# Kernel optimization log

Hardware: AMD Instinct MI355X
Metric: run time of the kernel (lower is better)

## Reference

```python
import jax, jax.numpy as jnp
import numpy as np

N_HEAD = 16
INPUT_DIM = 1024
D_K = 64


def setup_inputs() -> dict:
    key = jax.random.key(0)
    k1, k2, k3 = jax.random.split(key, 3)
    x = jax.random.normal(k1, (4, 2048, INPUT_DIM), dtype=jnp.float32)
    # xavier_uniform for linear weights
    def xavier(k, shape):
        fan_out, fan_in = shape
        limit = (6.0 / (fan_in + fan_out)) ** 0.5
        return jax.random.uniform(k, shape, jnp.float32, -limit, limit)
    W_qkv = xavier(k2, (3 * D_K * N_HEAD, INPUT_DIM))
    b_qkv = jnp.zeros((3 * D_K * N_HEAD,), jnp.float32)
    W_o = xavier(k3, (D_K * N_HEAD, D_K * N_HEAD))
    b_o = jnp.zeros((D_K * N_HEAD,), jnp.float32)
    return {"x": x, "W_qkv": W_qkv, "b_qkv": b_qkv, "W_o": W_o, "b_o": b_o}


def reference(x, W_qkv, b_qkv, W_o, b_o):
    B, S, _ = x.shape
    h = x @ W_qkv.T + b_qkv                      # (B, S, 3*d_k*H)
    # NOTE: original module reshapes directly (no transpose) to (B, H, S, 3*d_k)
    h = h.reshape(B, N_HEAD, S, 3 * D_K)
    q, k, v = jnp.split(h, 3, axis=-1)           # each (B, H, S, d_k)
    scores = jnp.einsum("bhqd,bhkd->bhqk", q, k) / jnp.sqrt(jnp.float32(D_K))
    attn = jax.nn.softmax(scores, axis=-1)       # (B, H, S, S)
    o = jnp.einsum("bhqk,bhkd->bhqd", attn, v)   # (B, H, S, d_k)
    o = o.transpose(0, 2, 1, 3).reshape(B, S, N_HEAD * D_K)
    return o @ W_o.T + b_o
```

## Files before the change

### kernel.cpp

```cpp
#include <hip/hip_runtime.h>
#include <stdint.h>


typedef __attribute__((ext_vector_type(8))) short short8;
typedef __attribute__((ext_vector_type(4))) short short4v;
typedef __attribute__((ext_vector_type(4))) float f32x4;
typedef __attribute__((ext_vector_type(16))) float f32x16;

#define B_SZ 4
#define S_SZ 2048
#define H_N 16
#define DK 64
#define IN_DIM 1024
#define QKV_DIM 3072
#define MODEL 1024
#define M_ROWS (B_SZ * S_SZ)

#define QSCALE 0.1803368801f

#if __has_builtin(__builtin_amdgcn_exp2f)
#define EXP2(x) __builtin_amdgcn_exp2f(x)
#else
#define EXP2(x) exp2f(x)
#endif

__device__ __forceinline__ short f2bf(float f) {
    union { float f; uint32_t u; } v; v.f = f;
    uint32_t r = v.u + 0x7FFFu + ((v.u >> 16) & 1u);
    return (short)(r >> 16);
}

__device__ __forceinline__ uint32_t pk2f(float a, float b) {
    uint32_t r;
    asm("v_cvt_pk_bf16_f32 %0, %1, %2" : "=v"(r) : "v"(a), "v"(b));
    return r;
}

__device__ __forceinline__ void gld_lds16(const void* g, void* l) {
    __builtin_amdgcn_global_load_lds(
        (const __attribute__((address_space(1))) void*)g,
        (__attribute__((address_space(3))) void*)l, 16, 0, 0);
}

__global__ __launch_bounds__(256) void cvt_kernel(
    const float* __restrict__ x, const float* __restrict__ wq,
    const float* __restrict__ wo, short* __restrict__ xb,
    short* __restrict__ wqb, short* __restrict__ wob) {
    const int NX = M_ROWS * IN_DIM / 4;
    const int NQ = QKV_DIM * IN_DIM / 4;
    const int NO = MODEL * IN_DIM / 4;
    const int total = NX + NQ + NO;
    for (int i = blockIdx.x * blockDim.x + threadIdx.x; i < total;
         i += gridDim.x * blockDim.x) {
        const f32x4* src; short4v* dst; int j;
        if (i < NX)           { src = (const f32x4*)x;  dst = (short4v*)xb;  j = i; }
        else if (i < NX + NQ) { src = (const f32x4*)wq; dst = (short4v*)wqb; j = i - NX; }
        else                  { src = (const f32x4*)wo; dst = (short4v*)wob; j = i - NX - NQ; }
        f32x4 v = src[j];
        short4v o;
        o[0] = f2bf(v[0]); o[1] = f2bf(v[1]); o[2] = f2bf(v[2]); o[3] = f2bf(v[3]);
        dst[j] = o;
    }
}

__global__ __launch_bounds__(512, 1) void gemm_big(
    const short* __restrict__ A, const short* __restrict__ Bm,
    const float* __restrict__ bias,
    short* __restrict__ Qb, short* __restrict__ Kb, short* __restrict__ Vt,
    int M, int N, int K) {
    __shared__ short As[4][256 * 32];
    __shared__ short Bs[4][256 * 32];
    const int tid = threadIdx.x;
    const int wave = tid >> 6, lane = tid & 63;
    const int row16 = lane & 15, kgrp = lane >> 4;
    const int wrbase = (wave >> 2) * 128;
    const int wcbase = (wave & 3) * 64;
    const int nwg = gridDim.x * gridDim.y;
    const int id = blockIdx.y * gridDim.x + blockIdx.x;
    const int nid = (id & 7) * (nwg >> 3) + (id >> 3);
    const int bn = nid % gridDim.x, bm = nid / gridDim.x;
    const short* Ab = A + (size_t)bm * 256 * K;
    const short* Bb = Bm + (size_t)bn * 256 * K;
    f32x4 acc[8][4] = {};

    const int srow = wave * 16 + (lane >> 2);
    const int soff = ((lane & 3) ^ ((lane >> 3) & 3)) * 8;
    const short* ag0 = Ab + (size_t)srow * K + soff;
    const short* ag1 = Ab + (size_t)(srow + 128) * K + soff;
    const short* bg0 = Bb + (size_t)srow * K + soff;
    const short* bg1 = Bb + (size_t)(srow + 128) * K + soff;
#define GSTAGE(BUF, K0)                                                        \
    {                                                                          \
        gld_lds16(ag0 + (K0), &As[BUF][(wave * 16) * 32]);                     \
        gld_lds16(ag1 + (K0), &As[BUF][(wave * 16 + 128) * 32]);               \
        gld_lds16(bg0 + (K0), &Bs[BUF][(wave * 16) * 32]);                     \
        gld_lds16(bg1 + (K0), &Bs[BUF][(wave * 16 + 128) * 32]);               \
    }
    const int NK = K >> 5;
    GSTAGE(0, 0);
    GSTAGE(1, 32);
    GSTAGE(2, 64);
    const int rch = (kgrp ^ ((row16 >> 1) & 3)) * 8;
    for (int t = 0; t < NK; ++t) {
        if (t + 2 < NK)      asm volatile("s_waitcnt vmcnt(8)" ::: "memory");
        else if (t + 1 < NK) asm volatile("s_waitcnt vmcnt(4)" ::: "memory");
        else                 asm volatile("s_waitcnt vmcnt(0)" ::: "memory");
        __builtin_amdgcn_s_barrier();
        __builtin_amdgcn_sched_barrier(0);
        const int cur = t & 3;
        const int nb = (t + 3) & 3;
        if (t + 3 < NK) {
            gld_lds16(ag0 + (t + 3) * 32, &As[nb][(wave * 16) * 32]);
            gld_lds16(ag1 + (t + 3) * 32, &As[nb][(wave * 16 + 128) * 32]);
        }
        short8 bf[4];
#pragma unroll
        for (int j = 0; j < 4; ++j)
            bf[j] = *(const short8*)&Bs[cur][(wcbase + j * 16 + row16) * 32 + rch];
        __builtin_amdgcn_s_setprio(1);
#pragma unroll
        for (int i = 0; i < 4; ++i) {
            short8 af = *(const short8*)&As[cur][(wrbase + i * 16 + row16) * 32 + rch];
#pragma unroll
            for (int j = 0; j < 4; ++j)
                acc[i][j] = __builtin_amdgcn_mfma_f32_16x16x32_bf16(
                    af, bf[j], acc[i][j], 0, 0, 0);
        }
        __builtin_amdgcn_s_setprio(0);
        if (t + 3 < NK) {
            gld_lds16(bg0 + (t + 3) * 32, &Bs[nb][(wave * 16) * 32]);
            gld_lds16(bg1 + (t + 3) * 32, &Bs[nb][(wave * 16 + 128) * 32]);
        }
        __builtin_amdgcn_s_setprio(1);
#pragma unroll
        for (int i = 4; i < 8; ++i) {
            short8 af = *(const short8*)&As[cur][(wrbase + i * 16 + row16) * 32 + rch];
#pragma unroll
            for (int j = 0; j < 4; ++j)
                acc[i][j] = __builtin_amdgcn_mfma_f32_16x16x32_bf16(
                    af, bf[j], acc[i][j], 0, 0, 0);
        }
        __builtin_amdgcn_s_setprio(0);
    }
#undef GSTAGE
#pragma unroll
    for (int j = 0; j < 4; ++j) {
        int gcol = bn * 256 + wcbase + j * 16 + row16;
        float bv = bias[gcol];
#pragma unroll
        for (int i = 0; i < 8; ++i) {
#pragma unroll
            for (int r = 0; r < 4; ++r) {
                int grow = bm * 256 + wrbase + i * 16 + kgrp * 4 + r;
                float val = acc[i][j][r] + bv;
                int b = grow >> 11, so = grow & 2047;
                int hh = so >> 7, a = so & 127;
                int rr = gcol / 192, cc = gcol - rr * 192;
                int ss = a * 16 + rr;
                int bh = b * H_N + hh;
                if (cc < 64) {
                    Qb[(((size_t)bh) * S_SZ + ss) * DK + cc] = f2bf(val * QSCALE);
                } else if (cc < 128) {
                    Kb[(((size_t)bh) * S_SZ + ss) * DK + cc - 64] = f2bf(val);
                } else {
                    Vt[((size_t)bh * DK + (cc - 128)) * S_SZ + ss] = f2bf(val);
                }
            }
        }
    }
}

template <int MODE>
__global__ __launch_bounds__(256, 2) void gemm_bt(
    const short* __restrict__ A, const short* __restrict__ Bm,
    const float* __restrict__ bias, float* __restrict__ Cout,
    short* __restrict__ Qb, short* __restrict__ Kb, short* __restrict__ Vt,
    int M, int N, int K) {
    __shared__ short As[3][128 * 32];
    __shared__ short Bs[3][128 * 32];
    const int tid = threadIdx.x;
    const int wave = tid >> 6, lane = tid & 63;
    const int row16 = lane & 15, kgrp = lane >> 4;
    const int wm = (wave >> 1) * 64, wn = (wave & 1) * 64;
    const int nwg = gridDim.x * gridDim.y;
    const int id = blockIdx.y * gridDim.x + blockIdx.x;
    const int nid = (id & 7) * (nwg >> 3) + (id >> 3);
    const int bn = nid % gridDim.x, bm = nid / gridDim.x;
    const short* Ab = A + (size_t)bm * 128 * K;
    const short* Bb = Bm + (size_t)bn * 128 * K;
    f32x4 acc[4][4] = {};

    const int srow = wave * 16 + (lane >> 2);
    const int soff = ((lane & 3) ^ ((srow >> 1) & 3)) * 8;
    const short* ag0 = Ab + (size_t)srow * K + soff;
    const short* ag1 = Ab + (size_t)(srow + 64) * K + soff;
    const short* bg0 = Bb + (size_t)srow * K + soff;
    const short* bg1 = Bb + (size_t)(srow + 64) * K + soff;
#define GSTAGE(BUF, K0)                                                        \
    {                                                                          \
        gld_lds16(ag0 + (K0), &As[BUF][(wave * 16) * 32]);                     \
        gld_lds16(ag1 + (K0), &As[BUF][(wave * 16 + 64) * 32]);                \
        gld_lds16(bg0 + (K0), &Bs[BUF][(wave * 16) * 32]);                     \
        gld_lds16(bg1 + (K0), &Bs[BUF][(wave * 16 + 64) * 32]);                \
    }

    const int NK = K >> 5;
    GSTAGE(0, 0);
    GSTAGE(1, 32);
    const int rch = (kgrp ^ ((row16 >> 1) & 3)) * 8;
    int cur = 0;
    for (int t = 0; t < NK; ++t) {
        if (t + 1 < NK) asm volatile("s_waitcnt vmcnt(4)" ::: "memory");
        else            asm volatile("s_waitcnt vmcnt(0)" ::: "memory");
        __builtin_amdgcn_s_barrier();
        __builtin_amdgcn_sched_barrier(0);
        if (t + 2 < NK) {
            int nb = cur + 2; if (nb >= 3) nb -= 3;
            GSTAGE(nb, (t + 2) * 32);
        }
        short8 af[4], bfr[4];
#pragma unroll
        for (int i = 0; i < 4; ++i)
            af[i] = *(const short8*)&As[cur][(wm + i * 16 + row16) * 32 + rch];
#pragma unroll
        for (int j = 0; j < 4; ++j)
            bfr[j] = *(const short8*)&Bs[cur][(wn + j * 16 + row16) * 32 + rch];
        __builtin_amdgcn_s_setprio(1);
#pragma unroll
        for (int i = 0; i < 4; ++i)
#pragma unroll
            for (int j = 0; j < 4; ++j)
                acc[i][j] = __builtin_amdgcn_mfma_f32_16x16x32_bf16(
                    af[i], bfr[j], acc[i][j], 0, 0, 0);
        __builtin_amdgcn_s_setprio(0);
        ++cur; if (cur == 3) cur = 0;
    }
#undef GSTAGE
#pragma unroll
    for (int j = 0; j < 4; ++j) {
        int gcol = bn * 128 + wn + j * 16 + row16;
        float bv = bias[gcol];
#pragma unroll
        for (int i = 0; i < 4; ++i) {
#pragma unroll
            for (int r = 0; r < 4; ++r) {
                int grow = bm * 128 + wm + i * 16 + kgrp * 4 + r;
                float val = acc[i][j][r] + bv;
                if (MODE == 1) {
                    Cout[(size_t)grow * N + gcol] = val;
                } else {
                    int b = grow >> 11, so = grow & 2047;
                    int hh = so >> 7, a = so & 127;
                    int rr = gcol / 192, cc = gcol - rr * 192;
                    int ss = a * 16 + rr;
                    int bh = b * H_N + hh;
                    if (cc < 64) {
                        Qb[(((size_t)bh) * S_SZ + ss) * DK + cc] = f2bf(val * QSCALE);
                    } else if (cc < 128) {
                        Kb[(((size_t)bh) * S_SZ + ss) * DK + cc - 64] = f2bf(val);
                    } else {
                        Vt[((size_t)bh * DK + (cc - 128)) * S_SZ + ss] = f2bf(val);
                    }
                }
            }
        }
    }
}

__global__ __launch_bounds__(256, 3) void attn_kernel(
    const short* __restrict__ Qg, const short* __restrict__ Kg,
    const short* __restrict__ Vtg, short* __restrict__ O) {
    __shared__ short Ks[2][64 * 64];
    __shared__ short Vs[2][64 * 64];
    const int tid = threadIdx.x;
    const int wave = tid >> 6, lane = tid & 63;
    const int q = lane & 31, hi = lane >> 5;
    const int id = blockIdx.x;
    const int bh = (id & 7) * 8 + ((id >> 3) & 7);
    const int qt = id >> 6;
    const int b = bh >> 4, h = bh & 15;
    const short* Qp = Qg + (size_t)bh * S_SZ * DK;
    const short* Kp = Kg + (size_t)bh * S_SZ * DK;
    const short* Vp = Vtg + (size_t)bh * DK * S_SZ;
    const int q0 = qt * 128 + wave * 32;

    short8 qf[4];
#pragma unroll
    for (int c = 0; c < 4; ++c)
        qf[c] = *(const short8*)&Qp[(size_t)(q0 + q) * DK + c * 16 + hi * 8];

    f32x16 ot0 = {}, ot1 = {};
    float m_run = -1e30f, l_run = 0.f;

    const int srow0 = wave * 16 + (lane >> 3);
    const int srow1 = srow0 + 8;
    const int sc0 = ((lane & 7) ^ (srow0 & 7)) * 8;
    const int sc1 = ((lane & 7) ^ (srow1 & 7)) * 8;
    const short* kg0 = Kp + (size_t)srow0 * DK + sc0;
    const short* kg1 = Kp + (size_t)srow1 * DK + sc1;
    const short* vg0 = Vp + (size_t)srow0 * S_SZ + sc0;
    const short* vg1 = Vp + (size_t)srow1 * S_SZ + sc1;
#define STAGE(BUF)                                                              \
    {                                                                           \
        gld_lds16(kg0, &Ks[BUF][(wave * 16) * 64]);                             \
        gld_lds16(kg1, &Ks[BUF][(wave * 16 + 8) * 64]);                         \
        gld_lds16(vg0, &Vs[BUF][(wave * 16) * 64]);                             \
        gld_lds16(vg1, &Vs[BUF][(wave * 16 + 8) * 64]);                         \
        kg0 += 64 * DK; kg1 += 64 * DK; vg0 += 64; vg1 += 64;                   \
    }

    STAGE(0);

    const int NT = S_SZ / 64;
    for (int t = 0; t < NT; ++t) {
        __syncthreads();
        const int cur = t & 1;
        if (t + 1 < NT) STAGE(cur ^ 1);

        const int qx = (q & 7) << 3;
        f32x16 st0 = {}, st1 = {};
        __builtin_amdgcn_s_setprio(1);
#pragma unroll
        for (int c = 0; c < 4; ++c) {
            const int sw = (((c * 2 + hi) << 3) ^ qx);
            short8 kf0 = *(const short8*)&Ks[cur][q * 64 + sw];
            short8 kf1 = *(const short8*)&Ks[cur][(32 + q) * 64 + sw];
            st0 = __builtin_amdgcn_mfma_f32_32x32x16_bf16(kf0, qf[c], st0, 0, 0, 0);
            st1 = __builtin_amdgcn_mfma_f32_32x32x16_bf16(kf1, qf[c], st1, 0, 0, 0);
        }
        __builtin_amdgcn_s_setprio(0);

        float ma = fmaxf(fmaxf(st0[0], st0[1]), st0[2]);
        float mb = fmaxf(fmaxf(st0[8], st0[9]), st0[10]);
        float mc = fmaxf(fmaxf(st1[0], st1[1]), st1[2]);
        float md = fmaxf(fmaxf(st1[8], st1[9]), st1[10]);
        ma = fmaxf(fmaxf(ma, st0[3]), st0[4]);
        mb = fmaxf(fmaxf(mb, st0[11]), st0[12]);
        mc = fmaxf(fmaxf(mc, st1[3]), st1[4]);
        md = fmaxf(fmaxf(md, st1[11]), st1[12]);
        ma = fmaxf(fmaxf(ma, st0[5]), st0[6]);
        mb = fmaxf(fmaxf(mb, st0[13]), st0[14]);
        mc = fmaxf(fmaxf(mc, st1[5]), st1[6]);
        md = fmaxf(fmaxf(md, st1[13]), st1[14]);
        ma = fmaxf(ma, st0[7]);
        mb = fmaxf(mb, st0[15]);
        mc = fmaxf(mc, st1[7]);
        md = fmaxf(md, st1[15]);
        float pm = fmaxf(fmaxf(ma, mb), fmaxf(mc, md));
        pm = fmaxf(pm, __shfl_xor(pm, 32));
        if (__any(pm > m_run + 8.f)) {
            float mnew = fmaxf(m_run, pm);
            float corr = EXP2(m_run - mnew);
            m_run = mnew;
            l_run *= corr;
#pragma unroll
            for (int r = 0; r < 16; ++r) { ot0[r] *= corr; ot1[r] *= corr; }
        }
        float s0 = 0.f, s1 = 0.f, s2 = 0.f, s3 = 0.f;
#pragma unroll
        for (int r = 0; r < 16; r += 4) {
            st0[r] = EXP2(st0[r] - m_run);         s0 += st0[r];
            st0[r + 1] = EXP2(st0[r + 1] - m_run); s1 += st0[r + 1];
            st0[r + 2] = EXP2(st0[r + 2] - m_run); s2 += st0[r + 2];
            st0[r + 3] = EXP2(st0[r + 3] - m_run); s3 += st0[r + 3];
        }
#pragma unroll
        for (int r = 0; r < 16; r += 4) {
            st1[r] = EXP2(st1[r] - m_run);         s0 += st1[r];
            st1[r + 1] = EXP2(st1[r + 1] - m_run); s1 += st1[r + 1];
            st1[r + 2] = EXP2(st1[r + 2] - m_run); s2 += st1[r + 2];
            st1[r + 3] = EXP2(st1[r + 3] - m_run); s3 += st1[r + 3];
        }
        float ssum = (s0 + s1) + (s2 + s3);
        ssum += __shfl_xor(ssum, 32);
        l_run += ssum;

        __builtin_amdgcn_s_setprio(1);
#if __has_builtin(__builtin_amdgcn_permlane32_swap)
#define PVCHUNK(ST, B0, CH)                                                    \
    {                                                                          \
        uint32_t A01 = pk2f(ST[(B0) + 0], ST[(B0) + 1]);                       \
        uint32_t A23 = pk2f(ST[(B0) + 2], ST[(B0) + 3]);                       \
        uint32_t B45 = pk2f(ST[(B0) + 4], ST[(B0) + 5]);                       \
        uint32_t B67 = pk2f(ST[(B0) + 6], ST[(B0) + 7]);                       \
        auto sw0 = __builtin_amdgcn_permlane32_swap(A01, B45, false, false);   \
        auto sw1 = __builtin_amdgcn_permlane32_swap(A23, B67, false, false);   \
        union { uint32_t u[4]; short8 s8; } pbu;                               \
        pbu.u[0] = sw0[0]; pbu.u[1] = sw1[0];                                  \
        pbu.u[2] = sw0[1]; pbu.u[3] = sw1[1];                                  \
        const int vsw = ((((CH) * 2 + hi) << 3) ^ qx);                         \
        short8 vf0 = *(const short8*)&Vs[cur][q * 64 + vsw];                   \
        short8 vf1 = *(const short8*)&Vs[cur][(32 + q) * 64 + vsw];            \
        ot0 = __builtin_amdgcn_mfma_f32_32x32x16_bf16(vf0, pbu.s8, ot0, 0, 0, 0); \
        ot1 = __builtin_amdgcn_mfma_f32_32x32x16_bf16(vf1, pbu.s8, ot1, 0, 0, 0); \
    }
#else
#define PVCHUNK(ST, B0, CH)                                                    \
    {                                                                          \
        uint32_t A01 = pk2f(ST[(B0) + 0], ST[(B0) + 1]);                       \
        uint32_t A23 = pk2f(ST[(B0) + 2], ST[(B0) + 3]);                       \
        uint32_t B45 = pk2f(ST[(B0) + 4], ST[(B0) + 5]);                       \
        uint32_t B67 = pk2f(ST[(B0) + 6], ST[(B0) + 7]);                       \
        uint32_t t0 = hi ? A01 : B45, t1 = hi ? A23 : B67;                     \
        uint32_t r0 = (uint32_t)__shfl_xor((int)t0, 32);                       \
        uint32_t r1 = (uint32_t)__shfl_xor((int)t1, 32);                       \
        union { uint32_t u[4]; short8 s8; } pbu;                               \
        pbu.u[0] = hi ? r0 : A01; pbu.u[1] = hi ? r1 : A23;                    \
        pbu.u[2] = hi ? B45 : r0; pbu.u[3] = hi ? B67 : r1;                    \
        const int vsw = ((((CH) * 2 + hi) << 3) ^ qx);                         \
        short8 vf0 = *(const short8*)&Vs[cur][q * 64 + vsw];                   \
        short8 vf1 = *(const short8*)&Vs[cur][(32 + q) * 64 + vsw];            \
        ot0 = __builtin_amdgcn_mfma_f32_32x32x16_bf16(vf0, pbu.s8, ot0, 0, 0, 0); \
        ot1 = __builtin_amdgcn_mfma_f32_32x32x16_bf16(vf1, pbu.s8, ot1, 0, 0, 0); \
    }
#endif
        PVCHUNK(st0, 0, 0);
        PVCHUNK(st0, 8, 1);
        PVCHUNK(st1, 0, 2);
        PVCHUNK(st1, 8, 3);
#undef PVCHUNK
        __builtin_amdgcn_s_setprio(0);
    }
#undef STAGE

    float inv = 1.f / l_run;
    size_t rowbase = ((size_t)b * S_SZ + (q0 + q)) * MODEL + h * DK;
#pragma unroll
    for (int i = 0; i < 4; ++i) {
        short4v v0, v1;
#pragma unroll
        for (int jj = 0; jj < 4; ++jj) {
            v0[jj] = f2bf(ot0[4 * i + jj] * inv);
            v1[jj] = f2bf(ot1[4 * i + jj] * inv);
        }
        *(short4v*)&O[rowbase + 8 * i + 4 * hi] = v0;
        *(short4v*)&O[rowbase + 32 + 8 * i + 4 * hi] = v1;
    }
}

extern "C" void kernel_launch(void* const* d_in, const int* in_sizes, int n_in,
                              void* d_out, int out_size, void* d_ws, size_t ws_size,
                              hipStream_t stream) {
    const float* x    = (const float*)d_in[0];
    const float* Wqkv = (const float*)d_in[1];
    const float* bqkv = (const float*)d_in[2];
    const float* Wo   = (const float*)d_in[3];
    const float* bo   = (const float*)d_in[4];
    float* out = (float*)d_out;
    char* ws = (char*)d_ws;

    short* xb  = (short*)(ws + 0);
    short* wqb = (short*)(ws + 16777216);
    short* wob = (short*)(ws + 23068672);
    short* Qb  = (short*)(ws + 25165824);
    short* Kb  = (short*)(ws + 41943040);
    short* Vt  = (short*)(ws + 58720256);
    short* Ob  = (short*)(ws + 0);

    cvt_kernel<<<dim3(2048), dim3(256), 0, stream>>>(x, Wqkv, Wo, xb, wqb, wob);
    gemm_big<<<dim3(QKV_DIM / 256, M_ROWS / 256), dim3(512), 0, stream>>>(
        xb, wqb, bqkv, Qb, Kb, Vt, M_ROWS, QKV_DIM, IN_DIM);
    attn_kernel<<<dim3(1024), dim3(256), 0, stream>>>(Qb, Kb, Vt, Ob);
    gemm_bt<1><<<dim3(MODEL / 128, M_ROWS / 128), dim3(256), 0, stream>>>(
        Ob, wob, bo, out, nullptr, nullptr, nullptr, M_ROWS, MODEL, IN_DIM);
}
```

Baseline: 248.2 us.

## Switch QKV GEMM to double-buffered BK=64 tiles with simple barrier pipeline

Rewrites the QKV projection GEMM main loop. It moves from a 4-stage BK=32 LDS ring with fine-grained vmcnt waits and split A/B prefetch to a 2-stage BK=64 double buffer with a full __syncthreads per iteration and an 8-chunk XOR swizzle. The aim is to halve the number of loop iterations and barriers per K and to simplify scheduling. The cost is a shallower prefetch depth (one tile ahead) and heavier full-block barriers, so global load latency may be less well hidden.

```diff
diff --git a/kernel.cpp b/kernel.cpp
--- a/kernel.cpp
+++ b/kernel.cpp
@@ -68,8 +68,8 @@
     const float* __restrict__ bias,
     short* __restrict__ Qb, short* __restrict__ Kb, short* __restrict__ Vt,
     int M, int N, int K) {
-    __shared__ short As[4][256 * 32];
-    __shared__ short Bs[4][256 * 32];
+    __shared__ short As[2][256 * 64];
+    __shared__ short Bs[2][256 * 64];
     const int tid = threadIdx.x;
     const int wave = tid >> 6, lane = tid & 63;
     const int row16 = lane & 15, kgrp = lane >> 4;
@@ -83,64 +83,48 @@
     const short* Bb = Bm + (size_t)bn * 256 * K;
     f32x4 acc[8][4] = {};
 
-    const int srow = wave * 16 + (lane >> 2);
-    const int soff = ((lane & 3) ^ ((lane >> 3) & 3)) * 8;
-    const short* ag0 = Ab + (size_t)srow * K + soff;
-    const short* ag1 = Ab + (size_t)(srow + 128) * K + soff;
-    const short* bg0 = Bb + (size_t)srow * K + soff;
-    const short* bg1 = Bb + (size_t)(srow + 128) * K + soff;
+    const int soff = ((lane & 7) ^ (lane >> 3)) * 8;
+    const int srow = wave * 8 + (lane >> 3);
 #define GSTAGE(BUF, K0)                                                        \
     {                                                                          \
-        gld_lds16(ag0 + (K0), &As[BUF][(wave * 16) * 32]);                     \
-        gld_lds16(ag1 + (K0), &As[BUF][(wave * 16 + 128) * 32]);               \
-        gld_lds16(bg0 + (K0), &Bs[BUF][(wave * 16) * 32]);                     \
-        gld_lds16(bg1 + (K0), &Bs[BUF][(wave * 16 + 128) * 32]);               \
-    }
-    const int NK = K >> 5;
+        _Pragma("unroll") for (int l = 0; l < 4; ++l) {                        \
+            gld_lds16(Ab + (size_t)(srow + l * 64) * K + (K0) + soff,          \
+                      &As[BUF][(wave * 8 + l * 64) * 64]);                     \
+            gld_lds16(Bb + (size_t)(srow + l * 64) * K + (K0) + soff,         \
+                      &Bs[BUF][(wave * 8 + l * 64) * 64]);                     \
+        }                                                                      \
+    }
+    const int NK = K >> 6;
     GSTAGE(0, 0);
-    GSTAGE(1, 32);
-    GSTAGE(2, 64);
-    const int rch = (kgrp ^ ((row16 >> 1) & 3)) * 8;
+    __syncthreads();
+    int cur = 0;
     for (int t = 0; t < NK; ++t) {
-        if (t + 2 < NK)      asm volatile("s_waitcnt vmcnt(8)" ::: "memory");
-        else if (t + 1 < NK) asm volatile("s_waitcnt vmcnt(4)" ::: "memory");
-        else                 asm volatile("s_waitcnt vmcnt(0)" ::: "memory");
-        __builtin_amdgcn_s_barrier();
-        __builtin_amdgcn_sched_barrier(0);
-        const int cur = t & 3;
-        const int nb = (t + 3) & 3;
-        if (t + 3 < NK) {
-            gld_lds16(ag0 + (t + 3) * 32, &As[nb][(wave * 16) * 32]);
-            gld_lds16(ag1 + (t + 3) * 32, &As[nb][(wave * 16 + 128) * 32]);
-        }
-        short8 bf[4];
-#pragma unroll
-        for (int j = 0; j < 4; ++j)
-            bf[j] = *(const short8*)&Bs[cur][(wcbase + j * 16 + row16) * 32 + rch];
+        if (t + 1 < NK) GSTAGE(cur ^ 1, (t + 1) * 64);
+        short8 bf[4][2];
+#pragma unroll
+        for (int j = 0; j < 4; ++j) {
+            int R = wcbase + j * 16 + row16;
+#pragma unroll
+            for (int kk = 0; kk < 2; ++kk)
+                bf[j][kk] = *(const short8*)
+                    &Bs[cur][R * 64 + (((kk * 4 + kgrp) ^ (R & 7)) * 8)];
+        }
         __builtin_amdgcn_s_setprio(1);
 #pragma unroll
-        for (int i = 0; i < 4; ++i) {
-            short8 af = *(const short8*)&As[cur][(wrbase + i * 16 + row16) * 32 + rch];
-#pragma unroll
-            for (int j = 0; j < 4; ++j)
-                acc[i][j] = __builtin_amdgcn_mfma_f32_16x16x32_bf16(
-                    af, bf[j], acc[i][j], 0, 0, 0);
-        }
+        for (int kk = 0; kk < 2; ++kk)
+#pragma unroll
+            for (int i = 0; i < 8; ++i) {
+                int R = wrbase + i * 16 + row16;
+                short8 af = *(const short8*)
+                    &As[cur][R * 64 + (((kk * 4 + kgrp) ^ (R & 7)) * 8)];
+#pragma unroll
+                for (int j = 0; j < 4; ++j)
+                    acc[i][j] = __builtin_amdgcn_mfma_f32_16x16x32_bf16(
+                        af, bf[j][kk], acc[i][j], 0, 0, 0);
+            }
         __builtin_amdgcn_s_setprio(0);
-        if (t + 3 < NK) {
-            gld_lds16(bg0 + (t + 3) * 32, &Bs[nb][(wave * 16) * 32]);
-            gld_lds16(bg1 + (t + 3) * 32, &Bs[nb][(wave * 16 + 128) * 32]);
-        }
-        __builtin_amdgcn_s_setprio(1);
-#pragma unroll
-        for (int i = 4; i < 8; ++i) {
-            short8 af = *(const short8*)&As[cur][(wrbase + i * 16 + row16) * 32 + rch];
-#pragma unroll
-            for (int j = 0; j < 4; ++j)
-                acc[i][j] = __builtin_amdgcn_mfma_f32_16x16x32_bf16(
-                    af, bf[j], acc[i][j], 0, 0, 0);
-        }
-        __builtin_amdgcn_s_setprio(0);
+        __syncthreads();
+        cur ^= 1;
     }
 #undef GSTAGE
 #pragma unroll
```

Result: no change. 246.2 us (-0.8%).
